# Kernel optimization log

Measured on AMD Instinct MI355X. Metric: run time of the kernel, lower is better.

The kernel has to match this reference:

```python
import jax, jax.numpy as jnp
import numpy as np

B, S, H, DH = 2, 4096, 8, 64
D = H * DH  # 512

def setup_inputs() -> dict:
    key = jax.random.key(0)
    ks = jax.random.split(key, 9)
    sc = 1.0 / np.sqrt(D)
    return {
        "hidden_states": jax.random.normal(ks[0], (B, S, D), jnp.float32),
        "Wq": jax.random.normal(ks[1], (D, D), jnp.float32) * sc,
        "bq": jax.random.normal(ks[2], (D,), jnp.float32) * 0.02,
        "Wk": jax.random.normal(ks[3], (D, D), jnp.float32) * sc,
        "bk": jax.random.normal(ks[4], (D,), jnp.float32) * 0.02,
        "Wv": jax.random.normal(ks[5], (D, D), jnp.float32) * sc,
        "bv": jax.random.normal(ks[6], (D,), jnp.float32) * 0.02,
        "Wo": jax.random.normal(ks[7], (D, D), jnp.float32) * sc,
        "bo": jax.random.normal(ks[8], (D,), jnp.float32) * 0.02,
    }

def _split_heads(t):
    # (B, S, H*DH) -> (B, H, S, DH)
    b = t.shape[0]
    return t.reshape(b, S, H, DH).transpose(0, 2, 1, 3)

def reference(hidden_states, Wq, bq, Wk, bk, Wv, bv, Wo, bo):
    q = _split_heads(hidden_states @ Wq + bq)
    k = _split_heads(hidden_states @ Wk + bk)
    v = _split_heads(hidden_states @ Wv + bv)
    scale = 1.0 / jnp.sqrt(jnp.asarray(DH, q.dtype))
    energy = jnp.einsum('bhqd,bhkd->bhqk', q, k) * scale
    weights = jax.nn.softmax(energy, axis=-1)  # full O(S^2) matrix, as in source
    attended = jnp.einsum('bhqv,bhvd->bhqd', weights, v)
    merged = attended.transpose(0, 2, 1, 3).reshape(hidden_states.shape[0], S, D)
    return merged @ Wo + bo
```

## Files before the change

kernel.cpp:

```cpp
#include <hip/hip_runtime.h>
#include <cstdint>

typedef __bf16 bf16;
typedef __bf16 bf16x4 __attribute__((ext_vector_type(4)));
typedef __bf16 bf16x8 __attribute__((ext_vector_type(8)));
typedef float floatx4 __attribute__((ext_vector_type(4)));

#define MFMA32(a, b, c) __builtin_amdgcn_mfma_f32_16x16x32_bf16((a), (b), (c), 0, 0, 0)

__device__ inline bf16x8 cvt8(const float* p) {
    float4 u = *(const float4*)p;
    float4 v = *(const float4*)(p + 4);
    bf16x8 r;
    r[0] = (bf16)u.x; r[1] = (bf16)u.y; r[2] = (bf16)u.z; r[3] = (bf16)u.w;
    r[4] = (bf16)v.x; r[5] = (bf16)v.y; r[6] = (bf16)v.z; r[7] = (bf16)v.w;
    return r;
}

__global__ __launch_bounds__(256) void k_prep(
    const float* __restrict__ X, bf16* __restrict__ Xb,
    const float* __restrict__ w0, const float* __restrict__ w1,
    const float* __restrict__ w2, const float* __restrict__ w3,
    bf16* __restrict__ o0, bf16* __restrict__ o1,
    bf16* __restrict__ o2, bf16* __restrict__ o3)
{
    __shared__ float t[32][33];
    const int bid = blockIdx.x;
    if (bid >= 1024) {
        const size_t idx = ((size_t)(bid - 1024) * 256 + threadIdx.x) * 8;
        *(bf16x8*)(Xb + idx) = cvt8(X + idx);
        return;
    }
    const float* in;
    bf16* out;
    switch (bid >> 8) {
        case 0: in = w0; out = o0; break;
        case 1: in = w1; out = o1; break;
        case 2: in = w2; out = o2; break;
        default: in = w3; out = o3; break;
    }
    const int tx = threadIdx.x & 31;
    const int ty = threadIdx.x >> 5;
    const int r0 = ((bid >> 4) & 15) * 32;
    const int c0 = (bid & 15) * 32;
    #pragma unroll
    for (int i = 0; i < 32; i += 8)
        t[ty + i][tx] = in[(size_t)(r0 + ty + i) * 512 + c0 + tx];
    __syncthreads();
    #pragma unroll
    for (int i = 0; i < 32; i += 8)
        out[(size_t)(c0 + ty + i) * 512 + r0 + tx] = (bf16)t[tx][ty + i];
}

__global__ __launch_bounds__(256) void k_qkv(
    const bf16* __restrict__ Xb, const bf16* __restrict__ Wcat,
    const float* __restrict__ bq, const float* __restrict__ bk, const float* __restrict__ bv,
    bf16* __restrict__ Qs, bf16* __restrict__ Ks, bf16* __restrict__ Vt)
{
    __shared__ __align__(16) unsigned char smem[36864];
    uint4* Al = (uint4*)smem;
    uint4* Bl = (uint4*)(smem + 16384);

    const int tid  = threadIdx.x;
    const int w    = tid >> 6;
    const int lane = tid & 63;
    const int col  = lane & 15;
    const int quad = lane >> 4;
    const int m0 = blockIdx.x * 128;
    const int n0 = blockIdx.y * 128;

    const bf16* gA0 = Xb   + (size_t)(m0 + (tid >> 2)) * 512 + (tid & 3) * 8;
    const bf16* gA1 = gA0 + 64 * 512;
    const bf16* gB0 = Wcat + (size_t)(n0 + (tid >> 2)) * 512 + (tid & 3) * 8;
    const bf16* gB1 = gB0 + 64 * 512;

    const floatx4 zf = {0.f, 0.f, 0.f, 0.f};
    floatx4 acc[4][4];
    #pragma unroll
    for (int a = 0; a < 4; ++a)
        #pragma unroll
        for (int b = 0; b < 4; ++b) acc[a][b] = zf;

    Al[tid]       = *(const uint4*)gA0;
    Al[tid + 256] = *(const uint4*)gA1;
    Bl[tid]       = *(const uint4*)gB0;
    Bl[tid + 256] = *(const uint4*)gB1;
    __syncthreads();

    const int mb = (w & 1) * 64;
    const int nb = (w >> 1) * 64;

    int buf = 0;
    for (int kk = 0; kk < 16; ++kk) {
        const int kn = ((kk + 1) & 15) * 32;
        const uint4 pa0 = *(const uint4*)(gA0 + kn);
        const uint4 pa1 = *(const uint4*)(gA1 + kn);
        const uint4 pb0 = *(const uint4*)(gB0 + kn);
        const uint4 pb1 = *(const uint4*)(gB1 + kn);

        const uint4* A4 = Al + buf * 512;
        const uint4* B4 = Bl + buf * 512;
        bf16x8 af[4], bfr[4];
        #pragma unroll
        for (int t = 0; t < 4; ++t) {
            union { uint4 u; bf16x8 v; } ca, cb;
            ca.u = A4[(mb + 16 * t + col) * 4 + quad];
            cb.u = B4[(nb + 16 * t + col) * 4 + quad];
            af[t] = ca.v;
            bfr[t] = cb.v;
        }
        #pragma unroll
        for (int tm = 0; tm < 4; ++tm)
            #pragma unroll
            for (int tn = 0; tn < 4; ++tn)
                acc[tm][tn] = MFMA32(af[tm], bfr[tn], acc[tm][tn]);

        const int nbuf = buf ^ 1;
        Al[nbuf * 512 + tid]       = pa0;
        Al[nbuf * 512 + tid + 256] = pa1;
        Bl[nbuf * 512 + tid]       = pb0;
        Bl[nbuf * 512 + tid + 256] = pb1;
        __syncthreads();
        buf = nbuf;
    }

    bf16* ep = (bf16*)smem + (size_t)w * 64 * 72;

    const int which = blockIdx.y >> 2;
    const int nbase = (blockIdx.y & 3) * 128 + nb;
    const int h  = nbase >> 6;
    const int mw = m0 + mb;
    const int b  = mw >> 12;
    const int s0 = mw & 4095;
    const float qsc = 0.125f * 1.44269504088896f;

    if (which == 2) {
        #pragma unroll
        for (int tn = 0; tn < 4; ++tn) {
            const int d = 16 * tn + col;
            const float bb = bv[nbase + d];
            #pragma unroll
            for (int tm = 0; tm < 4; ++tm) {
                union { bf16 e[4]; uint2 u; } pk;
                #pragma unroll
                for (int r = 0; r < 4; ++r) pk.e[r] = (bf16)(acc[tm][tn][r] + bb);
                *(uint2*)(ep + d * 72 + 16 * tm + 4 * quad) = pk.u;
            }
        }
    } else {
        const float* bias = (which == 0) ? bq : bk;
        const float sc = (which == 0) ? qsc : 1.0f;
        #pragma unroll
        for (int tn = 0; tn < 4; ++tn) {
            const int d = 16 * tn + col;
            const float bb = bias[nbase + d];
            #pragma unroll
            for (int tm = 0; tm < 4; ++tm)
                #pragma unroll
                for (int r = 0; r < 4; ++r)
                    ep[(16 * tm + 4 * quad + r) * 72 + d] = (bf16)((acc[tm][tn][r] + bb) * sc);
        }
    }

    asm volatile("" ::: "memory");

    const int rl = lane >> 3;
    const int ch = lane & 7;
    bf16* gbase;
    size_t rowstride;
    if (which == 2) {
        gbase = Vt + (((size_t)b * 8 + h) * 64) * 4096 + s0;
        rowstride = 4096;
    } else {
        bf16* P = (which == 0) ? Qs : Ks;
        gbase = P + (((size_t)b * 8 + h) * 4096 + s0) * 64;
        rowstride = 64;
    }
    #pragma unroll
    for (int it = 0; it < 8; ++it) {
        const int row = it * 8 + rl;
        const uint4 v = *(const uint4*)(ep + row * 72 + ch * 8);
        *(uint4*)(gbase + (size_t)row * rowstride + ch * 8) = v;
    }
}

__global__ __launch_bounds__(512, 2) void k_attn(
    const bf16* __restrict__ Qs, const bf16* __restrict__ Ks, const bf16* __restrict__ Vt,
    bf16* __restrict__ att)
{
    __shared__ __align__(16) unsigned char smem[33280];
    uint4* Klds = (uint4*)smem;
    uint4* Vlds = (uint4*)(smem + 16384);
    float* Of   = (float*)smem;
    float* Ls   = (float*)(smem + 32768);

    const int tid  = threadIdx.x;
    const int w    = tid >> 6;
    const int qt   = w >> 1;
    const int wq   = w & 1;
    const int lane = tid & 63;
    const int col  = lane & 15;
    const int quad = lane >> 4;
    const int i    = blockIdx.x;
    const int bh   = ((i & 7) << 1) | ((i >> 3) & 1);
    const int q0   = (i >> 4) * 128 + wq * 64;

    const bf16* Qb = Qs + (size_t)bh * 262144;
    const bf16* Kb = Ks + (size_t)bh * 262144 + (size_t)qt * 1024 * 64;
    const bf16* Vb = Vt + (size_t)bh * 262144 + (size_t)qt * 1024;

    const int t7  = tid & 127;
    const int rK  = t7 >> 3;
    const int lcK = (t7 & 7) ^ (rK & 7);
    const bf16* gK = Kb + (size_t)rK * 64 + lcK * 8;
    const int pV  = t7 >> 3;
    const int ccV = (t7 & 7) ^ (pV & 7);
    const int dV  = 2 * pV + (ccV >> 2);
    const int cV  = ccV & 3;
    const bf16* gV = Vb + (size_t)dV * 4096 + cV * 8;

    uint4* Kl2 = Klds + qt * 256;
    uint4* Vl2 = Vlds + qt * 256;

    bf16x8 aq[4][2];
    #pragma unroll
    for (int s = 0; s < 4; ++s)
        #pragma unroll
        for (int c = 0; c < 2; ++c)
            aq[s][c] = *(const bf16x8*)(Qb + (size_t)(q0 + 16 * s + col) * 64 + 32 * c + quad * 8);

    const floatx4 zf = {0.f, 0.f, 0.f, 0.f};
    floatx4 o[4][4];
    float lsum[4] = {0.f, 0.f, 0.f, 0.f};
    #pragma unroll
    for (int s = 0; s < 4; ++s)
        #pragma unroll
        for (int dt = 0; dt < 4; ++dt) o[s][dt] = zf;

    const int c1 = col & 1, ch2 = col >> 1, qh = quad >> 1, ql = quad & 1;

    Kl2[t7]       = *(const uint4*)gK;
    Kl2[t7 + 128] = *(const uint4*)(gK + 1024);
    Vl2[t7]       = *(const uint4*)gV;
    Vl2[t7 + 128] = *(const uint4*)(gV + 131072);
    __syncthreads();

    for (int kt = 0; kt < 1024; kt += 32) {
        const int kn = (kt + 32) & 1023;
        const uint4 kr0 = *(const uint4*)(gK + (size_t)kn * 64);
        const uint4 kr1 = *(const uint4*)(gK + (size_t)kn * 64 + 1024);
        const uint4 vr0 = *(const uint4*)(gV + kn);
        const uint4 vr1 = *(const uint4*)(gV + kn + 131072);

        const uint4* Kl = Kl2;
        const uint2* Vl = (const uint2*)Vl2;

        bf16x8 kf[2][2];
        #pragma unroll
        for (int t = 0; t < 2; ++t)
            #pragma unroll
            for (int c = 0; c < 2; ++c) {
                union { uint4 u; bf16x8 v; } cv;
                cv.u = Kl[(16 * t + col) * 8 + ((quad + 4 * c) ^ (col & 7))];
                kf[t][c] = cv.v;
            }
        bf16x8 vfrag8[4];
        #pragma unroll
        for (int dt = 0; dt < 4; ++dt) {
            union { uint2 u[2]; bf16x8 v; } cv;
            #pragma unroll
            for (int t = 0; t < 2; ++t) {
                const int slot = (dt * 8 + ch2) * 8 + ((c1 * 4 + 2 * t + qh) ^ ch2);
                cv.u[t] = Vl[slot * 2 + ql];
            }
            vfrag8[dt] = cv.v;
        }

        #pragma unroll
        for (int s = 0; s < 4; ++s) {
            union { bf16 e[8]; bf16x8 v; } pw;
            #pragma unroll
            for (int t = 0; t < 2; ++t) {
                floatx4 sc = MFMA32(kf[t][1], aq[s][1], MFMA32(kf[t][0], aq[s][0], zf));
                const float p0 = __builtin_amdgcn_exp2f(sc[0]);
                const float p1 = __builtin_amdgcn_exp2f(sc[1]);
                const float p2 = __builtin_amdgcn_exp2f(sc[2]);
                const float p3 = __builtin_amdgcn_exp2f(sc[3]);
                lsum[s] += (p0 + p1) + (p2 + p3);
                pw.e[4 * t + 0] = (bf16)p0; pw.e[4 * t + 1] = (bf16)p1;
                pw.e[4 * t + 2] = (bf16)p2; pw.e[4 * t + 3] = (bf16)p3;
            }
            #pragma unroll
            for (int dt = 0; dt < 4; ++dt)
                o[s][dt] = MFMA32(vfrag8[dt], pw.v, o[s][dt]);
        }

        __syncthreads();
        Kl2[t7]       = kr0;
        Kl2[t7 + 128] = kr1;
        Vl2[t7]       = vr0;
        Vl2[t7 + 128] = vr1;
        __syncthreads();
    }

    float lv[4];
    #pragma unroll
    for (int s = 0; s < 4; ++s) {
        float v = lsum[s];
        v += __shfl_xor(v, 16, 64);
        v += __shfl_xor(v, 32, 64);
        lv[s] = v;
    }

    float* opw = Of + (size_t)wq * 4096 + (size_t)lane * 64;

    __syncthreads();
    if (qt == 2) {
        #pragma unroll
        for (int s = 0; s < 4; ++s)
            #pragma unroll
            for (int dt = 0; dt < 4; ++dt)
                *(floatx4*)(opw + ((s * 4 + dt + lane) & 15) * 4) = o[s][dt];
        if (quad == 0) {
            #pragma unroll
            for (int s = 0; s < 4; ++s) Ls[(wq * 4 + s) * 16 + col] = lv[s];
        }
    }
    __syncthreads();
    if (qt == 0) {
        #pragma unroll
        for (int s = 0; s < 4; ++s) {
            #pragma unroll
            for (int dt = 0; dt < 4; ++dt)
                o[s][dt] += *(const floatx4*)(opw + ((s * 4 + dt + lane) & 15) * 4);
            lv[s] += Ls[(wq * 4 + s) * 16 + col];
        }
    }
    __syncthreads();
    if (qt == 3) {
        #pragma unroll
        for (int s = 0; s < 4; ++s)
            #pragma unroll
            for (int dt = 0; dt < 4; ++dt)
                *(floatx4*)(opw + ((s * 4 + dt + lane) & 15) * 4) = o[s][dt];
        if (quad == 0) {
            #pragma unroll
            for (int s = 0; s < 4; ++s) Ls[(wq * 4 + s) * 16 + col] = lv[s];
        }
    }
    __syncthreads();
    if (qt == 1) {
        #pragma unroll
        for (int s = 0; s < 4; ++s) {
            #pragma unroll
            for (int dt = 0; dt < 4; ++dt) {
                o[s][dt] += *(const floatx4*)(opw + ((s * 4 + dt + lane) & 15) * 4);
                *(floatx4*)(opw + ((s * 4 + dt + lane) & 15) * 4) = o[s][dt];
            }
            lv[s] += Ls[(wq * 4 + s) * 16 + col];
        }
        if (quad == 0) {
            #pragma unroll
            for (int s = 0; s < 4; ++s) Ls[(wq * 4 + s) * 16 + col] = lv[s];
        }
    }
    __syncthreads();
    if (qt == 0) {
        float inv[4];
        #pragma unroll
        for (int s = 0; s < 4; ++s)
            inv[s] = 1.0f / (lv[s] + Ls[(wq * 4 + s) * 16 + col]);
        const int b  = bh >> 3;
        const int hh = bh & 7;
        #pragma unroll
        for (int s = 0; s < 4; ++s)
            #pragma unroll
            for (int dt = 0; dt < 4; ++dt) {
                const floatx4 po = *(const floatx4*)(opw + ((s * 4 + dt + lane) & 15) * 4);
                union { bf16 e[4]; uint2 u; } pk;
                #pragma unroll
                for (int r = 0; r < 4; ++r)
                    pk.e[r] = (bf16)((o[s][dt][r] + po[r]) * inv[s]);
                const size_t row = (size_t)b * 4096 + q0 + 16 * s + col;
                *(uint2*)(att + row * 512 + hh * 64 + 16 * dt + 4 * quad) = pk.u;
            }
    }
}

__global__ __launch_bounds__(256) void k_oproj(
    const bf16* __restrict__ att, const bf16* __restrict__ Wto,
    const float* __restrict__ bo, float* __restrict__ out)
{
    __shared__ uint4 Al[2][512];
    __shared__ uint4 Bl[2][512];

    const int tid  = threadIdx.x;
    const int w    = tid >> 6;
    const int lane = tid & 63;
    const int col  = lane & 15;
    const int quad = lane >> 4;
    const int m0 = blockIdx.x * 128;
    const int n0 = blockIdx.y * 128;

    const bf16* gA0 = att + (size_t)(m0 + (tid >> 2)) * 512 + (tid & 3) * 8;
    const bf16* gA1 = gA0 + 64 * 512;
    const bf16* gB0 = Wto + (size_t)(n0 + (tid >> 2)) * 512 + (tid & 3) * 8;
    const bf16* gB1 = gB0 + 64 * 512;

    const floatx4 zf = {0.f, 0.f, 0.f, 0.f};
    floatx4 acc[4][4];
    #pragma unroll
    for (int a = 0; a < 4; ++a)
        #pragma unroll
        for (int b = 0; b < 4; ++b) acc[a][b] = zf;

    Al[0][tid]       = *(const uint4*)gA0;
    Al[0][tid + 256] = *(const uint4*)gA1;
    Bl[0][tid]       = *(const uint4*)gB0;
    Bl[0][tid + 256] = *(const uint4*)gB1;
    __syncthreads();

    const int mb = (w & 1) * 64;
    const int nb = (w >> 1) * 64;

    int buf = 0;
    for (int kk = 0; kk < 16; ++kk) {
        const int kn = ((kk + 1) & 15) * 32;
        const uint4 pa0 = *(const uint4*)(gA0 + kn);
        const uint4 pa1 = *(const uint4*)(gA1 + kn);
        const uint4 pb0 = *(const uint4*)(gB0 + kn);
        const uint4 pb1 = *(const uint4*)(gB1 + kn);

        const uint4* A4 = Al[buf];
        const uint4* B4 = Bl[buf];
        bf16x8 af[4], bfr[4];
        #pragma unroll
        for (int t = 0; t < 4; ++t) {
            union { uint4 u; bf16x8 v; } ca, cb;
            ca.u = A4[(mb + 16 * t + col) * 4 + quad];
            cb.u = B4[(nb + 16 * t + col) * 4 + quad];
            af[t] = ca.v;
            bfr[t] = cb.v;
        }
        #pragma unroll
        for (int tm = 0; tm < 4; ++tm)
            #pragma unroll
            for (int tn = 0; tn < 4; ++tn)
                acc[tm][tn] = MFMA32(af[tm], bfr[tn], acc[tm][tn]);

        Al[buf ^ 1][tid]       = pa0;
        Al[buf ^ 1][tid + 256] = pa1;
        Bl[buf ^ 1][tid]       = pb0;
        Bl[buf ^ 1][tid + 256] = pb1;
        __syncthreads();
        buf ^= 1;
    }

    #pragma unroll
    for (int tn = 0; tn < 4; ++tn) {
        const int n = n0 + nb + 16 * tn + col;
        const float bb = bo[n];
        #pragma unroll
        for (int tm = 0; tm < 4; ++tm)
            #pragma unroll
            for (int r = 0; r < 4; ++r) {
                const int m = m0 + mb + 16 * tm + quad * 4 + r;
                out[(size_t)m * 512 + n] = acc[tm][tn][r] + bb;
            }
    }
}

extern "C" void kernel_launch(void* const* d_in, const int* in_sizes, int n_in,
                              void* d_out, int out_size, void* d_ws, size_t ws_size,
                              hipStream_t stream)
{
    const float* X  = (const float*)d_in[0];
    const float* Wq = (const float*)d_in[1];
    const float* bq = (const float*)d_in[2];
    const float* Wk = (const float*)d_in[3];
    const float* bk = (const float*)d_in[4];
    const float* Wv = (const float*)d_in[5];
    const float* bv = (const float*)d_in[6];
    const float* Wo = (const float*)d_in[7];
    const float* bo = (const float*)d_in[8];

    bf16* Wtq = (bf16*)d_ws;
    bf16* Wtk = Wtq + 512 * 512;
    bf16* Wtv = Wtk + 512 * 512;
    bf16* Wto = Wtv + 512 * 512;
    bf16* Qs  = Wto + 512 * 512;
    bf16* Ks  = Qs + (size_t)16 * 4096 * 64;
    bf16* Vt  = Ks + (size_t)16 * 4096 * 64;
    bf16* att = Vt + (size_t)16 * 4096 * 64;

    bf16* Xb  = (bf16*)d_out;

    k_prep<<<3072, 256, 0, stream>>>(X, Xb, Wq, Wk, Wv, Wo, Wtq, Wtk, Wtv, Wto);
    k_qkv<<<dim3(64, 12), 256, 0, stream>>>(Xb, Wtq, bq, bk, bv, Qs, Ks, Vt);
    k_attn<<<512, 512, 0, stream>>>(Qs, Ks, Vt, att);
    k_oproj<<<dim3(64, 4), 256, 0, stream>>>(att, Wto, bo, (float*)d_out);
}
```

Baseline: 191.2 us.

## Use direct global-to-LDS loads in GEMMs and shrink oproj tiles

Replaces the register-staged prefetch in the QKV and output-projection GEMMs with global_load_lds 16-byte direct copies into the alternate LDS buffer, and drops the redundant wraparound load on the last iteration. The output projection is retiled from 128x128 to 64x64 blocks, giving 1024 blocks instead of 256 so the launch fills more compute units. The direct-to-LDS path avoids VGPR staging and the extra LDS store instructions. The cost is that each block now does less work per barrier, and the code relies on the barrier to make the asynchronous LDS writes visible.

```diff
diff --git a/kernel.cpp b/kernel.cpp
--- a/kernel.cpp
+++ b/kernel.cpp
@@ -7,6 +7,12 @@
 typedef float floatx4 __attribute__((ext_vector_type(4)));
 
 #define MFMA32(a, b, c) __builtin_amdgcn_mfma_f32_16x16x32_bf16((a), (b), (c), 0, 0, 0)
+
+__device__ inline void load_lds16(const void* g, void* l) {
+    __builtin_amdgcn_global_load_lds(
+        (const __attribute__((address_space(1))) void*)g,
+        (__attribute__((address_space(3))) void*)l, 16, 0, 0);
+}
 
 __device__ inline bf16x8 cvt8(const float* p) {
     float4 u = *(const float4*)p;
@@ -81,10 +87,10 @@
         #pragma unroll
         for (int b = 0; b < 4; ++b) acc[a][b] = zf;
 
-    Al[tid]       = *(const uint4*)gA0;
-    Al[tid + 256] = *(const uint4*)gA1;
-    Bl[tid]       = *(const uint4*)gB0;
-    Bl[tid + 256] = *(const uint4*)gB1;
+    load_lds16(gA0, &Al[tid]);
+    load_lds16(gA1, &Al[tid + 256]);
+    load_lds16(gB0, &Bl[tid]);
+    load_lds16(gB1, &Bl[tid + 256]);
     __syncthreads();
 
     const int mb = (w & 1) * 64;
@@ -92,12 +98,15 @@
 
     int buf = 0;
     for (int kk = 0; kk < 16; ++kk) {
-        const int kn = ((kk + 1) & 15) * 32;
-        const uint4 pa0 = *(const uint4*)(gA0 + kn);
-        const uint4 pa1 = *(const uint4*)(gA1 + kn);
-        const uint4 pb0 = *(const uint4*)(gB0 + kn);
-        const uint4 pb1 = *(const uint4*)(gB1 + kn);
-
+        if (kk < 15) {
+            const int kn = (kk + 1) * 32;
+            uint4* An = Al + (buf ^ 1) * 512;
+            uint4* Bn = Bl + (buf ^ 1) * 512;
+            load_lds16(gA0 + kn, &An[tid]);
+            load_lds16(gA1 + kn, &An[tid + 256]);
+            load_lds16(gB0 + kn, &Bn[tid]);
+            load_lds16(gB1 + kn, &Bn[tid + 256]);
+        }
         const uint4* A4 = Al + buf * 512;
         const uint4* B4 = Bl + buf * 512;
         bf16x8 af[4], bfr[4];
@@ -115,13 +124,8 @@
             for (int tn = 0; tn < 4; ++tn)
                 acc[tm][tn] = MFMA32(af[tm], bfr[tn], acc[tm][tn]);
 
-        const int nbuf = buf ^ 1;
-        Al[nbuf * 512 + tid]       = pa0;
-        Al[nbuf * 512 + tid + 256] = pa1;
-        Bl[nbuf * 512 + tid]       = pb0;
-        Bl[nbuf * 512 + tid + 256] = pb1;
         __syncthreads();
-        buf = nbuf;
+        buf ^= 1;
     }
 
     bf16* ep = (bf16*)smem + (size_t)w * 64 * 72;
@@ -391,51 +395,46 @@
     const bf16* __restrict__ att, const bf16* __restrict__ Wto,
     const float* __restrict__ bo, float* __restrict__ out)
 {
-    __shared__ uint4 Al[2][512];
-    __shared__ uint4 Bl[2][512];
+    __shared__ __align__(16) uint4 Al[2][256];
+    __shared__ __align__(16) uint4 Bl[2][256];
 
     const int tid  = threadIdx.x;
     const int w    = tid >> 6;
     const int lane = tid & 63;
     const int col  = lane & 15;
     const int quad = lane >> 4;
-    const int m0 = blockIdx.x * 128;
-    const int n0 = blockIdx.y * 128;
-
-    const bf16* gA0 = att + (size_t)(m0 + (tid >> 2)) * 512 + (tid & 3) * 8;
-    const bf16* gA1 = gA0 + 64 * 512;
-    const bf16* gB0 = Wto + (size_t)(n0 + (tid >> 2)) * 512 + (tid & 3) * 8;
-    const bf16* gB1 = gB0 + 64 * 512;
+    const int n0 = blockIdx.x * 64;
+    const int m0 = blockIdx.y * 64;
+
+    const bf16* gA = att + (size_t)(m0 + (tid >> 2)) * 512 + (tid & 3) * 8;
+    const bf16* gB = Wto + (size_t)(n0 + (tid >> 2)) * 512 + (tid & 3) * 8;
 
     const floatx4 zf = {0.f, 0.f, 0.f, 0.f};
-    floatx4 acc[4][4];
-    #pragma unroll
-    for (int a = 0; a < 4; ++a)
-        #pragma unroll
-        for (int b = 0; b < 4; ++b) acc[a][b] = zf;
-
-    Al[0][tid]       = *(const uint4*)gA0;
-    Al[0][tid + 256] = *(const uint4*)gA1;
-    Bl[0][tid]       = *(const uint4*)gB0;
-    Bl[0][tid + 256] = *(const uint4*)gB1;
-    __syncthreads();
-
-    const int mb = (w & 1) * 64;
-    const int nb = (w >> 1) * 64;
+    floatx4 acc[2][2];
+    #pragma unroll
+    for (int a = 0; a < 2; ++a)
+        #pragma unroll
+        for (int b = 0; b < 2; ++b) acc[a][b] = zf;
+
+    load_lds16(gA, &Al[0][tid]);
+    load_lds16(gB, &Bl[0][tid]);
+    __syncthreads();
+
+    const int mb = (w & 1) * 32;
+    const int nb = (w >> 1) * 32;
 
     int buf = 0;
     for (int kk = 0; kk < 16; ++kk) {
-        const int kn = ((kk + 1) & 15) * 32;
-        const uint4 pa0 = *(const uint4*)(gA0 + kn);
-        const uint4 pa1 = *(const uint4*)(gA1 + kn);
-        const uint4 pb0 = *(const uint4*)(gB0 + kn);
-        const uint4 pb1 = *(const uint4*)(gB1 + kn);
-
+        if (kk < 15) {
+            const int kn = (kk + 1) * 32;
+            load_lds16(gA + kn, &Al[buf ^ 1][tid]);
+            load_lds16(gB + kn, &Bl[buf ^ 1][tid]);
+        }
         const uint4* A4 = Al[buf];
         const uint4* B4 = Bl[buf];
-        bf16x8 af[4], bfr[4];
-        #pragma unroll
-        for (int t = 0; t < 4; ++t) {
+        bf16x8 af[2], bfr[2];
+        #pragma unroll
+        for (int t = 0; t < 2; ++t) {
             union { uint4 u; bf16x8 v; } ca, cb;
             ca.u = A4[(mb + 16 * t + col) * 4 + quad];
             cb.u = B4[(nb + 16 * t + col) * 4 + quad];
@@ -443,25 +442,21 @@
             bfr[t] = cb.v;
         }
         #pragma unroll
-        for (int tm = 0; tm < 4; ++tm)
-            #pragma unroll
-            for (int tn = 0; tn < 4; ++tn)
+        for (int tm = 0; tm < 2; ++tm)
+            #pragma unroll
+            for (int tn = 0; tn < 2; ++tn)
                 acc[tm][tn] = MFMA32(af[tm], bfr[tn], acc[tm][tn]);
 
-        Al[buf ^ 1][tid]       = pa0;
-        Al[buf ^ 1][tid + 256] = pa1;
-        Bl[buf ^ 1][tid]       = pb0;
-        Bl[buf ^ 1][tid + 256] = pb1;
         __syncthreads();
         buf ^= 1;
     }
 
     #pragma unroll
-    for (int tn = 0; tn < 4; ++tn) {
+    for (int tn = 0; tn < 2; ++tn) {
         const int n = n0 + nb + 16 * tn + col;
         const float bb = bo[n];
         #pragma unroll
-        for (int tm = 0; tm < 4; ++tm)
+        for (int tm = 0; tm < 2; ++tm)
             #pragma unroll
             for (int r = 0; r < 4; ++r) {
                 const int m = m0 + mb + 16 * tm + quad * 4 + r;
@@ -498,5 +493,5 @@
     k_prep<<<3072, 256, 0, stream>>>(X, Xb, Wq, Wk, Wv, Wo, Wtq, Wtk, Wtv, Wto);
     k_qkv<<<dim3(64, 12), 256, 0, stream>>>(Xb, Wtq, bq, bk, bv, Qs, Ks, Vt);
     k_attn<<<512, 512, 0, stream>>>(Qs, Ks, Vt, att);
-    k_oproj<<<dim3(64, 4), 256, 0, stream>>>(att, Wto, bo, (float*)d_out);
-}
+    k_oproj<<<dim3(8, 128), 256, 0, stream>>>(att, Wto, bo, (float*)d_out);
+}
```

Result: slower. 196.4 us (+2.7%).
